# Kernel optimization log

Hardware: AMD Instinct MI355X
Metric: run time of the kernel (lower is better)

## Reference

```python
import jax, jax.numpy as jnp
import numpy as np

SEQ, BATCH, IN, RES = 1024, 64, 512, 2048

def setup_inputs() -> dict:
    key = jax.random.key(0)
    k1, k2, k3, k4 = jax.random.split(key, 4)
    x = jax.random.normal(k1, (SEQ, BATCH, IN), dtype=jnp.float32)
    # ESN reservoir weights: untrained random matrices (spectral-radius style scaling)
    W_in = jax.random.normal(k2, (RES, IN), dtype=jnp.float32) * 0.1
    W_hh = jax.random.normal(k3, (RES, RES), dtype=jnp.float32) * (0.9 / jnp.sqrt(RES))
    b = jax.random.normal(k4, (RES,), dtype=jnp.float32) * 0.1
    return {"x": x, "W_in": W_in, "W_hh": W_hh, "b": b}

def reference(x, W_in, W_hh, b):
    # ESNBase.forward -> _forward_type_2 with num_layers=1, unidirectional.
    # h_t = tanh(x_t @ W_in^T + h_{t-1} @ W_hh^T + b)
    batch = x.shape[1]
    h0 = jnp.zeros((batch, W_hh.shape[0]), dtype=x.dtype)
    # Precompute input projection for all steps (parallel GEMM), scan the recurrence.
    xin = jnp.einsum('sbi,ri->sbr', x, W_in) + b  # (seq, batch, res)
    def step(h, u):
        h_new = jnp.tanh(u + h @ W_hh.T)
        return h_new, h_new
    h_n, states = jax.lax.scan(step, h0, xin)
    # output: (seq, batch, num_directions*hidden); h_n: (num_layers*num_directions, batch, hidden)
    return states, h_n[None, :, :]
```

## Files before the change

### kernel.cpp

```cpp
#include <hip/hip_runtime.h>
#include <hip/hip_bf16.h>


#define SEQ  1024
#define NB   64
#define INF  512
#define RES  2048
#define RING 16

typedef float    f32x4 __attribute__((ext_vector_type(4)));
typedef _Float16 f16x8 __attribute__((ext_vector_type(8)));

__device__ __forceinline__ float fast_tanh(float x) {
  const float e = __expf(2.0f * x);
  return 1.0f - 2.0f * __builtin_amdgcn_rcpf(1.0f + e);
}

__global__ __launch_bounds__(256) void xin_gemm(
    const float* __restrict__ X, const float* __restrict__ Win,
    const float* __restrict__ bias, float* __restrict__ U)
{
  __shared__ _Float16 lA[2][128][40];
  __shared__ _Float16 lB[2][128][40];

  const int tid  = threadIdx.x;
  const int lane = tid & 63;
  const int wv   = tid >> 6;
  const int wr   = wv >> 1;
  const int wc   = wv & 1;
  const int m0   = (blockIdx.x >> 4) * 128;
  const int n0   = (blockIdx.x & 15) * 128;

  const int srow = tid >> 1;
  const int sk   = (tid & 1) * 16;

  const int fr = lane & 15;
  const int fk = (lane >> 4) * 8;

  f32x4 acc[4][4] = {};
  float ra[16], rb[16];

  const float* xa_base = X   + (size_t)(m0 + srow) * INF + sk;
  const float* xb_base = Win + (size_t)(n0 + srow) * INF + sk;

#define LOADK(kt) do {                                                     \
    const float* pa = xa_base + (kt) * 32;                                 \
    const float* pb = xb_base + (kt) * 32;                                 \
    *(f32x4*)&ra[0]  = *(const f32x4*)(pa + 0);                            \
    *(f32x4*)&ra[4]  = *(const f32x4*)(pa + 4);                            \
    *(f32x4*)&ra[8]  = *(const f32x4*)(pa + 8);                            \
    *(f32x4*)&ra[12] = *(const f32x4*)(pa + 12);                           \
    *(f32x4*)&rb[0]  = *(const f32x4*)(pb + 0);                            \
    *(f32x4*)&rb[4]  = *(const f32x4*)(pb + 4);                            \
    *(f32x4*)&rb[8]  = *(const f32x4*)(pb + 8);                            \
    *(f32x4*)&rb[12] = *(const f32x4*)(pb + 12);                           \
  } while (0)

#define STOREK(buf) do {                                                   \
    f16x8 h0, h1;                                                          \
    _Pragma("unroll") for (int j = 0; j < 8; ++j) h0[j] = (_Float16)ra[j]; \
    _Pragma("unroll") for (int j = 0; j < 8; ++j) h1[j] = (_Float16)ra[8+j];\
    *(f16x8*)&lA[buf][srow][sk]     = h0;                                  \
    *(f16x8*)&lA[buf][srow][sk + 8] = h1;                                  \
    _Pragma("unroll") for (int j = 0; j < 8; ++j) h0[j] = (_Float16)rb[j]; \
    _Pragma("unroll") for (int j = 0; j < 8; ++j) h1[j] = (_Float16)rb[8+j];\
    *(f16x8*)&lB[buf][srow][sk]     = h0;                                  \
    *(f16x8*)&lB[buf][srow][sk + 8] = h1;                                  \
  } while (0)

#define COMPUTE(buf) do {                                                  \
    f16x8 af[4], bf[4];                                                    \
    _Pragma("unroll") for (int mt = 0; mt < 4; ++mt)                       \
      af[mt] = *(const f16x8*)&lA[buf][wr*64 + mt*16 + fr][fk];            \
    _Pragma("unroll") for (int nt = 0; nt < 4; ++nt)                       \
      bf[nt] = *(const f16x8*)&lB[buf][wc*64 + nt*16 + fr][fk];            \
    _Pragma("unroll") for (int mt = 0; mt < 4; ++mt)                       \
      _Pragma("unroll") for (int nt = 0; nt < 4; ++nt)                     \
        acc[mt][nt] = __builtin_amdgcn_mfma_f32_16x16x32_f16(              \
            af[mt], bf[nt], acc[mt][nt], 0, 0, 0);                         \
  } while (0)

  LOADK(0);
  STOREK(0);
  __syncthreads();

#pragma unroll 1
  for (int kt = 0; kt < 16; ++kt) {
    const int buf = kt & 1;
    if (kt < 15) LOADK(kt + 1);
    COMPUTE(buf);
    if (kt < 15) STOREK(buf ^ 1);
    __syncthreads();
  }

#pragma unroll
  for (int mt = 0; mt < 4; ++mt) {
    const int row = m0 + wr*64 + mt*16 + (lane >> 4) * 4;
#pragma unroll
    for (int nt = 0; nt < 4; ++nt) {
      const int col = n0 + wc*64 + nt*16 + fr;
      const float bv = bias[col];
#pragma unroll
      for (int i = 0; i < 4; ++i)
        U[(size_t)(row + i) * RES + col] = acc[mt][nt][i] + bv;
    }
  }
#undef LOADK
#undef STOREK
#undef COMPUTE
}

__global__ __launch_bounds__(512, 1) void esn_recur(
    const float* __restrict__ Whh, float* __restrict__ states,
    float* __restrict__ hn, _Float16* __restrict__ ring,
    unsigned* __restrict__ flags)
{
  __shared__ float red[8][32][17];

  const int tid  = threadIdx.x;
  const int lane = tid & 63;
  const int wv   = tid >> 6;
  const int q    = wv;

  const int bid = blockIdx.x;
  const int xg  = bid & 7;
  const int bg  = xg >> 1;
  const int cg  = ((xg & 1) << 5) | (bid >> 3);
  const int b0  = bg * 16;
  const int c0  = cg * 32;

  const int fr = lane & 15;
  const int fk = (lane >> 4) * 8;

  const int er = tid >> 5;
  const int ec = tid & 31;

  f16x8 wf[2][8];
#pragma unroll
  for (int t = 0; t < 2; ++t)
#pragma unroll
    for (int ks = 0; ks < 8; ++ks) {
      const float* src = Whh + (size_t)(c0 + t*16 + fr) * RES
                       + q*256 + ks*32 + fk;
      const f32x4 w0 = *(const f32x4*)src;
      const f32x4 w1 = *(const f32x4*)(src + 4);
      f16x8 f;
#pragma unroll
      for (int j = 0; j < 4; ++j) { f[j] = (_Float16)w0[j]; f[4+j] = (_Float16)w1[j]; }
      wf[t][ks] = f;
    }

  unsigned* const fb = flags + bg * (128 * 32);

  for (int s = 0; s < SEQ; ++s) {
    const float u = states[(size_t)s * NB * RES + (size_t)(b0 + er) * RES + c0 + ec];

    f32x4 a0 = {0.f, 0.f, 0.f, 0.f}, a1 = {0.f, 0.f, 0.f, 0.f};

    if (s > 0) {
      const _Float16* hp = ring + (size_t)((s - 1) & (RING - 1)) * (NB * RES)
                         + (size_t)(b0 + fr) * RES + q*256 + fk;
      f16x8 hv[8];
      for (;;) {
#pragma unroll
        for (int ks = 0; ks < 8; ++ks) {
          union { unsigned long long w[2]; f16x8 v; } au;
          au.w[0] = __hip_atomic_load((const unsigned long long*)(hp + ks*32),
                                      __ATOMIC_RELAXED, __HIP_MEMORY_SCOPE_AGENT);
          au.w[1] = __hip_atomic_load((const unsigned long long*)(hp + ks*32 + 4),
                                      __ATOMIC_RELAXED, __HIP_MEMORY_SCOPE_AGENT);
          hv[ks] = au.v;
        }
        const f16x8 ss = ((hv[0] + hv[1]) + (hv[2] + hv[3]))
                       + ((hv[4] + hv[5]) + (hv[6] + hv[7]));
        union { f16x8 v; unsigned w[4]; } su; su.v = ss;
        unsigned bad = 0;
#pragma unroll
        for (int j = 0; j < 4; ++j) {
          bad |= ((su.w[j] & 0x7C00u) == 0x7C00u);
          bad |= (((su.w[j] >> 16) & 0x7C00u) == 0x7C00u);
        }
        if (!__any(bad)) break;
      }
#pragma unroll
      for (int ks = 0; ks < 8; ++ks) {
        a0 = __builtin_amdgcn_mfma_f32_16x16x32_f16(hv[ks], wf[0][ks], a0, 0, 0, 0);
        a1 = __builtin_amdgcn_mfma_f32_16x16x32_f16(hv[ks], wf[1][ks], a1, 0, 0, 0);
      }
    }

    {
      const int r4 = (lane >> 4) * 4;
      float* d0 = &red[q][fr][r4];
      float* d1 = &red[q][16 + fr][r4];
#pragma unroll
      for (int i = 0; i < 4; ++i) { d0[i] = a0[i]; d1[i] = a1[i]; }
    }
    __syncthreads();

    float sum = u;
#pragma unroll
    for (int qq = 0; qq < 8; ++qq) sum += red[qq][ec][er];
    const float v = fast_tanh(sum);

    const size_t off = (size_t)(b0 + er) * RES + c0 + ec;
    states[(size_t)s * NB * RES + off] = v;
    {
      unsigned short* hc = (unsigned short*)(ring
                         + (size_t)(s & (RING - 1)) * (NB * RES));
      const unsigned short hb = __builtin_bit_cast(unsigned short, (_Float16)v);
      __hip_atomic_store(hc + off, hb,
                         __ATOMIC_RELAXED, __HIP_MEMORY_SCOPE_AGENT);
      if (s == SEQ - 1) hn[off] = v;
    }

    const bool barrier_step = ((s & 7) == 7) && (s != SEQ - 1);
    if (barrier_step) {
      if (wv < 2) {
        const int col = c0 + wv * 16 + fr;
#pragma unroll
        for (int d = 1; d <= 8; ++d) {
          unsigned short* pz = (unsigned short*)(ring
                             + (size_t)((s + d) & (RING - 1)) * (NB * RES));
#pragma unroll
          for (int i = 0; i < 4; ++i) {
            const size_t poff = (size_t)(b0 + (lane >> 4) * 4 + i) * RES + col;
            __hip_atomic_store(&pz[poff], (unsigned short)0x7F7Fu,
                               __ATOMIC_RELAXED, __HIP_MEMORY_SCOPE_AGENT);
          }
        }
        asm volatile("s_waitcnt vmcnt(0)" ::: "memory");
        if (lane == 0)
          __hip_atomic_store(fb + (wv * 64 + cg) * 32, (unsigned)((s >> 3) + 1),
                             __ATOMIC_RELAXED, __HIP_MEMORY_SCOPE_AGENT);
      } else if (wv == 2) {
        const unsigned tgt = (unsigned)((s >> 3) + 1);
        for (;;) {
          const unsigned va = __hip_atomic_load(fb + lane * 32,
                                __ATOMIC_RELAXED, __HIP_MEMORY_SCOPE_AGENT);
          const unsigned vb = __hip_atomic_load(fb + (64 + lane) * 32,
                                __ATOMIC_RELAXED, __HIP_MEMORY_SCOPE_AGENT);
          if (__all((va >= tgt) & (vb >= tgt))) break;
        }
      }
    }
    __syncthreads();
  }
}

extern "C" void kernel_launch(void* const* d_in, const int* in_sizes, int n_in,
                              void* d_out, int out_size, void* d_ws, size_t ws_size,
                              hipStream_t stream) {
  const float* x    = (const float*)d_in[0];
  const float* W_in = (const float*)d_in[1];
  const float* W_hh = (const float*)d_in[2];
  const float* bias = (const float*)d_in[3];

  float* states = (float*)d_out;
  float* hn     = states + (size_t)SEQ * NB * RES;

  _Float16* ring  = (_Float16*)d_ws;
  unsigned* flags = (unsigned*)((char*)d_ws
                  + (size_t)RING * NB * RES * sizeof(_Float16));

  hipMemsetAsync(ring, 0x7F, (size_t)RING * NB * RES * sizeof(_Float16), stream);
  hipMemsetAsync(flags, 0, (size_t)4 * 128 * 32 * sizeof(unsigned), stream);

  xin_gemm<<<dim3(512 * 16), dim3(256), 0, stream>>>(x, W_in, bias, states);
  esn_recur<<<dim3(256), dim3(512), 0, stream>>>(W_hh, states, hn, ring, flags);
}
```

Baseline: 6.746 ms.

## Fuse input projection GEMM into the persistent recurrence kernel

Removes the separate xin_gemm kernel and computes x_t @ W_in^T inside the recurrent kernel each step. Each block keeps its slice of W_in in registers as fp16 fragments and does 4 extra MFMAs per wave per step, adding the bias directly. This drops the full-size write and read of the precomputed projection through the states buffer, plus a kernel launch. The cost is more register pressure and extra x loads on the latency-bound serial critical path, although those loads do not depend on the previous step.

```diff
diff --git a/kernel.cpp b/kernel.cpp
--- a/kernel.cpp
+++ b/kernel.cpp
@@ -16,104 +16,11 @@
   return 1.0f - 2.0f * __builtin_amdgcn_rcpf(1.0f + e);
 }
 
-__global__ __launch_bounds__(256) void xin_gemm(
-    const float* __restrict__ X, const float* __restrict__ Win,
-    const float* __restrict__ bias, float* __restrict__ U)
-{
-  __shared__ _Float16 lA[2][128][40];
-  __shared__ _Float16 lB[2][128][40];
-
-  const int tid  = threadIdx.x;
-  const int lane = tid & 63;
-  const int wv   = tid >> 6;
-  const int wr   = wv >> 1;
-  const int wc   = wv & 1;
-  const int m0   = (blockIdx.x >> 4) * 128;
-  const int n0   = (blockIdx.x & 15) * 128;
-
-  const int srow = tid >> 1;
-  const int sk   = (tid & 1) * 16;
-
-  const int fr = lane & 15;
-  const int fk = (lane >> 4) * 8;
-
-  f32x4 acc[4][4] = {};
-  float ra[16], rb[16];
-
-  const float* xa_base = X   + (size_t)(m0 + srow) * INF + sk;
-  const float* xb_base = Win + (size_t)(n0 + srow) * INF + sk;
-
-#define LOADK(kt) do {                                                     \
-    const float* pa = xa_base + (kt) * 32;                                 \
-    const float* pb = xb_base + (kt) * 32;                                 \
-    *(f32x4*)&ra[0]  = *(const f32x4*)(pa + 0);                            \
-    *(f32x4*)&ra[4]  = *(const f32x4*)(pa + 4);                            \
-    *(f32x4*)&ra[8]  = *(const f32x4*)(pa + 8);                            \
-    *(f32x4*)&ra[12] = *(const f32x4*)(pa + 12);                           \
-    *(f32x4*)&rb[0]  = *(const f32x4*)(pb + 0);                            \
-    *(f32x4*)&rb[4]  = *(const f32x4*)(pb + 4);                            \
-    *(f32x4*)&rb[8]  = *(const f32x4*)(pb + 8);                            \
-    *(f32x4*)&rb[12] = *(const f32x4*)(pb + 12);                           \
-  } while (0)
-
-#define STOREK(buf) do {                                                   \
-    f16x8 h0, h1;                                                          \
-    _Pragma("unroll") for (int j = 0; j < 8; ++j) h0[j] = (_Float16)ra[j]; \
-    _Pragma("unroll") for (int j = 0; j < 8; ++j) h1[j] = (_Float16)ra[8+j];\
-    *(f16x8*)&lA[buf][srow][sk]     = h0;                                  \
-    *(f16x8*)&lA[buf][srow][sk + 8] = h1;                                  \
-    _Pragma("unroll") for (int j = 0; j < 8; ++j) h0[j] = (_Float16)rb[j]; \
-    _Pragma("unroll") for (int j = 0; j < 8; ++j) h1[j] = (_Float16)rb[8+j];\
-    *(f16x8*)&lB[buf][srow][sk]     = h0;                                  \
-    *(f16x8*)&lB[buf][srow][sk + 8] = h1;                                  \
-  } while (0)
-
-#define COMPUTE(buf) do {                                                  \
-    f16x8 af[4], bf[4];                                                    \
-    _Pragma("unroll") for (int mt = 0; mt < 4; ++mt)                       \
-      af[mt] = *(const f16x8*)&lA[buf][wr*64 + mt*16 + fr][fk];            \
-    _Pragma("unroll") for (int nt = 0; nt < 4; ++nt)                       \
-      bf[nt] = *(const f16x8*)&lB[buf][wc*64 + nt*16 + fr][fk];            \
-    _Pragma("unroll") for (int mt = 0; mt < 4; ++mt)                       \
-      _Pragma("unroll") for (int nt = 0; nt < 4; ++nt)                     \
-        acc[mt][nt] = __builtin_amdgcn_mfma_f32_16x16x32_f16(              \
-            af[mt], bf[nt], acc[mt][nt], 0, 0, 0);                         \
-  } while (0)
-
-  LOADK(0);
-  STOREK(0);
-  __syncthreads();
-
-#pragma unroll 1
-  for (int kt = 0; kt < 16; ++kt) {
-    const int buf = kt & 1;
-    if (kt < 15) LOADK(kt + 1);
-    COMPUTE(buf);
-    if (kt < 15) STOREK(buf ^ 1);
-    __syncthreads();
-  }
-
-#pragma unroll
-  for (int mt = 0; mt < 4; ++mt) {
-    const int row = m0 + wr*64 + mt*16 + (lane >> 4) * 4;
-#pragma unroll
-    for (int nt = 0; nt < 4; ++nt) {
-      const int col = n0 + wc*64 + nt*16 + fr;
-      const float bv = bias[col];
-#pragma unroll
-      for (int i = 0; i < 4; ++i)
-        U[(size_t)(row + i) * RES + col] = acc[mt][nt][i] + bv;
-    }
-  }
-#undef LOADK
-#undef STOREK
-#undef COMPUTE
-}
-
 __global__ __launch_bounds__(512, 1) void esn_recur(
-    const float* __restrict__ Whh, float* __restrict__ states,
-    float* __restrict__ hn, _Float16* __restrict__ ring,
-    unsigned* __restrict__ flags)
+    const float* __restrict__ X, const float* __restrict__ Whh,
+    const float* __restrict__ Win, const float* __restrict__ bias,
+    float* __restrict__ states, float* __restrict__ hn,
+    _Float16* __restrict__ ring, unsigned* __restrict__ flags)
 {
   __shared__ float red[8][32][17];
 
@@ -150,10 +57,35 @@
       wf[t][ks] = f;
     }
 
+  f16x8 winf[2][2];
+#pragma unroll
+  for (int t = 0; t < 2; ++t)
+#pragma unroll
+    for (int ks = 0; ks < 2; ++ks) {
+      const float* src = Win + (size_t)(c0 + t*16 + fr) * INF
+                       + q*64 + ks*32 + fk;
+      const f32x4 w0 = *(const f32x4*)src;
+      const f32x4 w1 = *(const f32x4*)(src + 4);
+      f16x8 f;
+#pragma unroll
+      for (int j = 0; j < 4; ++j) { f[j] = (_Float16)w0[j]; f[4+j] = (_Float16)w1[j]; }
+      winf[t][ks] = f;
+    }
+
+  const float bv = bias[c0 + ec];
+
   unsigned* const fb = flags + bg * (128 * 32);
 
   for (int s = 0; s < SEQ; ++s) {
-    const float u = states[(size_t)s * NB * RES + (size_t)(b0 + er) * RES + c0 + ec];
+    f32x4 xr0a, xr0b, xr1a, xr1b;
+    {
+      const float* xp = X + (size_t)s * (NB * INF)
+                      + (size_t)(b0 + fr) * INF + q*64 + fk;
+      xr0a = *(const f32x4*)(xp);
+      xr0b = *(const f32x4*)(xp + 4);
+      xr1a = *(const f32x4*)(xp + 32);
+      xr1b = *(const f32x4*)(xp + 36);
+    }
 
     f32x4 a0 = {0.f, 0.f, 0.f, 0.f}, a1 = {0.f, 0.f, 0.f, 0.f};
 
@@ -190,6 +122,19 @@
     }
 
     {
+      f16x8 xa0, xa1;
+#pragma unroll
+      for (int j = 0; j < 4; ++j) {
+        xa0[j] = (_Float16)xr0a[j]; xa0[4+j] = (_Float16)xr0b[j];
+        xa1[j] = (_Float16)xr1a[j]; xa1[4+j] = (_Float16)xr1b[j];
+      }
+      a0 = __builtin_amdgcn_mfma_f32_16x16x32_f16(xa0, winf[0][0], a0, 0, 0, 0);
+      a0 = __builtin_amdgcn_mfma_f32_16x16x32_f16(xa1, winf[0][1], a0, 0, 0, 0);
+      a1 = __builtin_amdgcn_mfma_f32_16x16x32_f16(xa0, winf[1][0], a1, 0, 0, 0);
+      a1 = __builtin_amdgcn_mfma_f32_16x16x32_f16(xa1, winf[1][1], a1, 0, 0, 0);
+    }
+
+    {
       const int r4 = (lane >> 4) * 4;
       float* d0 = &red[q][fr][r4];
       float* d1 = &red[q][16 + fr][r4];
@@ -198,7 +143,7 @@
     }
     __syncthreads();
 
-    float sum = u;
+    float sum = bv;
 #pragma unroll
     for (int qq = 0; qq < 8; ++qq) sum += red[qq][ec][er];
     const float v = fast_tanh(sum);
@@ -266,6 +211,6 @@
   hipMemsetAsync(ring, 0x7F, (size_t)RING * NB * RES * sizeof(_Float16), stream);
   hipMemsetAsync(flags, 0, (size_t)4 * 128 * 32 * sizeof(unsigned), stream);
 
-  xin_gemm<<<dim3(512 * 16), dim3(256), 0, stream>>>(x, W_in, bias, states);
-  esn_recur<<<dim3(256), dim3(512), 0, stream>>>(W_hh, states, hn, ring, flags);
+  esn_recur<<<dim3(256), dim3(512), 0, stream>>>(x, W_hh, W_in, bias,
+                                                 states, hn, ring, flags);
 }
```

Result: faster. 6.337 ms (-6.1%).
